# Kernel tuning notes

Measured on AMD Instinct MI355X. Metric: run time of the kernel, lower is better.

The kernel has to match this reference:

```python
import jax, jax.numpy as jnp
import numpy as np
from jax import lax

STRIDES = (8, 16, 32, 64, 128)
LEVEL_HW = ((100, 128), (50, 64), (25, 32), (13, 16), (7, 8))
NUM_CLASSES = 80
PRE_NMS_THRESH = 0.05
PRE_NMS_TOPK = 1000
NMS_THRESH = 0.6
MAX_DET = 100
CLS_OFFSET = 1.0e4  # > max image coordinate, separates classes for joint NMS


def setup_inputs() -> dict:
    key = jax.random.key(0)
    B = 16
    ks = jax.random.split(key, 3 * len(LEVEL_HW))
    inp = {}
    i = 0
    for lvl, (h, w) in enumerate(LEVEL_HW):
        # shift logits down so sigmoid scores are mostly below the 0.05 candidate
        # threshold (realistic detection sparsity)
        inp[f"logits_p{lvl + 3}"] = jax.random.normal(ks[i], (B, NUM_CLASSES, h, w), jnp.float32) - 4.0; i += 1
        inp[f"bbox_p{lvl + 3}"] = jax.random.uniform(ks[i], (B, 4, h, w), jnp.float32, minval=0.0, maxval=64.0); i += 1
        inp[f"ctr_p{lvl + 3}"] = jax.random.normal(ks[i], (B, 1, h, w), jnp.float32); i += 1
    inp["im_info"] = jnp.tile(jnp.array([[800.0, 1024.0]], jnp.float32), (B, 1))
    return inp


def _locations(h, w, stride):
    # FCOSLocation: center of each stride cell -> [HW, 2] as (x, y)
    sx = jnp.arange(w, dtype=jnp.float32) * stride + stride // 2
    sy = jnp.arange(h, dtype=jnp.float32) * stride + stride // 2
    yy, xx = jnp.meshgrid(sy, sx, indexing="ij")
    return jnp.stack([xx.reshape(-1), yy.reshape(-1)], axis=-1)


def _nms_single(boxes, scores, classes):
    # boxes [K,4], scores [K] (descending), classes [K] int
    off = classes.astype(jnp.float32)[:, None] * CLS_OFFSET
    nb = boxes + off  # class-offset trick -> per-class NMS in one pass
    areas = jnp.maximum(nb[:, 2] - nb[:, 0], 0.0) * jnp.maximum(nb[:, 3] - nb[:, 1], 0.0)

    def body(sc, _):
        i = jnp.argmax(sc)
        s = sc[i]
        bi = nb[i]
        xx1 = jnp.maximum(bi[0], nb[:, 0])
        yy1 = jnp.maximum(bi[1], nb[:, 1])
        xx2 = jnp.minimum(bi[2], nb[:, 2])
        yy2 = jnp.minimum(bi[3], nb[:, 3])
        inter = jnp.maximum(xx2 - xx1, 0.0) * jnp.maximum(yy2 - yy1, 0.0)
        iou = inter / (areas[i] + areas - inter + 1e-9)
        sc2 = jnp.where(iou >= NMS_THRESH, -jnp.inf, sc).at[i].set(-jnp.inf)
        return sc2, (i, s > 0.0)

    _, (idxs, valid) = lax.scan(body, scores, None, length=MAX_DET)
    det = jnp.concatenate(
        [boxes[idxs], scores[idxs][:, None], classes[idxs].astype(jnp.float32)[:, None]],
        axis=-1,
    )  # [MAX_DET, 6] = x1,y1,x2,y2,score,class
    return jnp.where(valid[:, None], det, 0.0)


def _forward(logits_p3, bbox_p3, ctr_p3, logits_p4, bbox_p4, ctr_p4,
             logits_p5, bbox_p5, ctr_p5, logits_p6, bbox_p6, ctr_p6,
             logits_p7, bbox_p7, ctr_p7, im_info):
    levels = [(logits_p3, bbox_p3, ctr_p3), (logits_p4, bbox_p4, ctr_p4),
              (logits_p5, bbox_p5, ctr_p5), (logits_p6, bbox_p6, ctr_p6),
              (logits_p7, bbox_p7, ctr_p7)]
    scores_l, boxes_l = [], []
    for (lg, rg, ct), stride in zip(levels, STRIDES):
        B, C, H, W = lg.shape
        cls = jax.nn.sigmoid(lg).transpose(0, 2, 3, 1).reshape(B, H * W, C)
        cen = jax.nn.sigmoid(ct).transpose(0, 2, 3, 1).reshape(B, H * W, 1)
        # candidate threshold on raw class prob, then modulate by centerness
        comb = jnp.where(cls > PRE_NMS_THRESH, cls * cen, 0.0)
        locs = _locations(H, W, stride)  # [HW, 2]
        reg = rg.transpose(0, 2, 3, 1).reshape(B, H * W, 4)  # (l, t, r, b)
        bx = jnp.stack([locs[None, :, 0] - reg[..., 0],
                        locs[None, :, 1] - reg[..., 1],
                        locs[None, :, 0] + reg[..., 2],
                        locs[None, :, 1] + reg[..., 3]], axis=-1)
        scores_l.append(comb)
        boxes_l.append(bx)
    scores = jnp.concatenate(scores_l, axis=1)  # [B, N, C]
    boxes = jnp.concatenate(boxes_l, axis=1)    # [B, N, 4]
    B, N, C = scores.shape
    vals, idx = lax.top_k(scores.reshape(B, N * C), PRE_NMS_TOPK)  # [B, K]
    loc = idx // C
    cls_id = idx % C
    cand = jnp.take_along_axis(boxes, loc[..., None], axis=1)  # [B, K, 4]
    h = im_info[:, 0:1]
    w = im_info[:, 1:2]
    x1 = jnp.clip(cand[..., 0], 0.0, w - 1.0)
    y1 = jnp.clip(cand[..., 1], 0.0, h - 1.0)
    x2 = jnp.clip(cand[..., 2], 0.0, w - 1.0)
    y2 = jnp.clip(cand[..., 3], 0.0, h - 1.0)
    cand = jnp.stack([x1, y1, x2, y2], axis=-1)
    sc = jnp.where(vals > 0.0, jnp.sqrt(jnp.maximum(vals, 0.0) + 1e-12), 0.0)
    return jax.vmap(_nms_single)(cand, sc, cls_id)  # [B, MAX_DET, 6]


def reference(logits_p3, bbox_p3, ctr_p3, logits_p4, bbox_p4, ctr_p4,
              logits_p5, bbox_p5, ctr_p5, logits_p6, bbox_p6, ctr_p6,
              logits_p7, bbox_p7, ctr_p7, im_info):
    return _forward(logits_p3, bbox_p3, ctr_p3, logits_p4, bbox_p4, ctr_p4,
                    logits_p5, bbox_p5, ctr_p5, logits_p6, bbox_p6, ctr_p6,
                    logits_p7, bbox_p7, ctr_p7, im_info)
```

## Files before the change

kernel.cpp:

```cpp
#include <hip/hip_runtime.h>
#include <math.h>

#pragma clang fp contract(off)

#define NB 16
#define NC 80
#define NTOT 17064
#define TOPK 1000
#define NBINS 8192
#define CAP 4096
#define MAXDET 100
#define CNTSTRIDE 64
#define CHUNK 128
#define GH 128
#define WSEGCAP 256
#define FB 16

struct Ptrs {
    const float* lg[5];
    const float* bb[5];
    const float* ct[5];
};

__device__ __forceinline__ void level_of(int n, int& l, int& hw, int& W,
                                         int& stride, int& half, int& HW) {
    if (n < 12800)      { l = 0; hw = n;         W = 128; stride = 8;   half = 4;  HW = 12800; }
    else if (n < 16000) { l = 1; hw = n - 12800; W = 64;  stride = 16;  half = 8;  HW = 3200;  }
    else if (n < 16800) { l = 2; hw = n - 16000; W = 32;  stride = 32;  half = 16; HW = 800;   }
    else if (n < 17008) { l = 3; hw = n - 16800; W = 16;  stride = 64;  half = 32; HW = 208;   }
    else                { l = 4; hw = n - 17008; W = 8;   stride = 128; half = 64; HW = 56;    }
}

__device__ __forceinline__ float fast_sig(float x) {
    float e = __expf(-x);
    return __builtin_amdgcn_rcpf(1.0f + e);
}

#define HG_EMIT(BITS, NN, CC, POS)                                            \
    {                                                                         \
        int lb = (int)(((BITS) - 32u) >> 19) - BINBASE;                       \
        lb = (lb < 0) ? 0 : ((lb > 63) ? 63 : lb);                            \
        atomicAdd(&whv[lb], 1u);             \
        unsigned pos_ = (POS);                                                \
        if (pos_ < WSEGCAP) {                                                 \
            unsigned idx_ = (unsigned)((NN) * NC + (CC));                     \
            segw[pos_] = ((unsigned long long)(BITS) << 32) | idx_;           \
        }                                                                     \
    }

#define LOADQ(I, V, C, HWV, CCV)                                              \
    V = make_float4(-40.f, -40.f, -40.f, -40.f);                              \
    C = make_float4(0.f, 0.f, 0.f, 0.f);                                      \
    HWV = 0; CCV = 0;                                                         \
    if ((I) < NF4) {                                                          \
        CCV = (I) / HW4; HWV = (I) - CCV * HW4;                               \
        V = *(const float4*)(lgb + (size_t)(I) * 4);                          \
        C = *(const float4*)(ctb + HWV * 4);                                  \
    }

template<int HW4, int NF4, int LVOFF>
__device__ __forceinline__ void histg_level(const float* lgb, const float* ctb,
        int tid, int bx, int gx, unsigned FB_LO, int BINBASE, unsigned* whv,
        unsigned& wcnt, unsigned long long* segw, unsigned long long ltmask) {
    const int stride = gx * 512;
    int i0 = bx * 512;
    if (i0 >= NF4) return;
    float4 va, vb, ca, cb;
    int hwa, hwb, cca, ccb;
    LOADQ(i0 + tid, va, ca, hwa, cca)
    LOADQ(i0 + 256 + tid, vb, cb, hwb, ccb)
    for (; i0 < NF4; ) {
        int in0 = i0 + stride;
        float4 nva, nvb, nca, ncb;
        int nhwa, nhwb, ncca, nccb;
        LOADQ(in0 + tid, nva, nca, nhwa, ncca)
        LOADQ(in0 + 256 + tid, nvb, ncb, nhwb, nccb)
        unsigned b0 = __float_as_uint(fast_sig(va.x) * fast_sig(ca.x));
        unsigned b1 = __float_as_uint(fast_sig(va.y) * fast_sig(ca.y));
        unsigned b2 = __float_as_uint(fast_sig(va.z) * fast_sig(ca.z));
        unsigned b3 = __float_as_uint(fast_sig(va.w) * fast_sig(ca.w));
        unsigned b4 = __float_as_uint(fast_sig(vb.x) * fast_sig(cb.x));
        unsigned b5 = __float_as_uint(fast_sig(vb.y) * fast_sig(cb.y));
        unsigned b6 = __float_as_uint(fast_sig(vb.z) * fast_sig(cb.z));
        unsigned b7 = __float_as_uint(fast_sig(vb.w) * fast_sig(cb.w));
        bool f0 = b0 >= FB_LO, f1 = b1 >= FB_LO, f2 = b2 >= FB_LO, f3 = b3 >= FB_LO;
        bool f4 = b4 >= FB_LO, f5 = b5 >= FB_LO, f6 = b6 >= FB_LO, f7 = b7 >= FB_LO;
        unsigned long long m0 = __ballot(f0), m1 = __ballot(f1);
        unsigned long long m2 = __ballot(f2), m3 = __ballot(f3);
        unsigned long long m4 = __ballot(f4), m5 = __ballot(f5);
        unsigned long long m6 = __ballot(f6), m7 = __ballot(f7);
        if (m0 | m1 | m2 | m3 | m4 | m5 | m6 | m7) {
            unsigned t0 = (unsigned)__popcll(m0), t1 = (unsigned)__popcll(m1);
            unsigned t2 = (unsigned)__popcll(m2), t3 = (unsigned)__popcll(m3);
            unsigned t4 = (unsigned)__popcll(m4), t5 = (unsigned)__popcll(m5);
            unsigned t6 = (unsigned)__popcll(m6), t7 = (unsigned)__popcll(m7);
            unsigned wb = wcnt;
            wcnt = wb + t0 + t1 + t2 + t3 + t4 + t5 + t6 + t7;
            int nb0a = LVOFF + hwa * 4, nb0b = LVOFF + hwb * 4;
            if (f0) HG_EMIT(b0, nb0a + 0, cca, wb + (unsigned)__popcll(m0 & ltmask))
            if (f1) HG_EMIT(b1, nb0a + 1, cca, wb + t0 + (unsigned)__popcll(m1 & ltmask))
            if (f2) HG_EMIT(b2, nb0a + 2, cca, wb + t0 + t1 + (unsigned)__popcll(m2 & ltmask))
            if (f3) HG_EMIT(b3, nb0a + 3, cca, wb + t0 + t1 + t2 + (unsigned)__popcll(m3 & ltmask))
            if (f4) HG_EMIT(b4, nb0b + 0, ccb, wb + t0 + t1 + t2 + t3 + (unsigned)__popcll(m4 & ltmask))
            if (f5) HG_EMIT(b5, nb0b + 1, ccb, wb + t0 + t1 + t2 + t3 + t4 + (unsigned)__popcll(m5 & ltmask))
            if (f6) HG_EMIT(b6, nb0b + 2, ccb, wb + t0 + t1 + t2 + t3 + t4 + t5 + (unsigned)__popcll(m6 & ltmask))
            if (f7) HG_EMIT(b7, nb0b + 3, ccb, wb + t0 + t1 + t2 + t3 + t4 + t5 + t6 + (unsigned)__popcll(m7 & ltmask))
        }
        i0 = in0;
        va = nva; ca = nca; hwa = nhwa; cca = ncca;
        vb = nvb; cb = ncb; hwb = nhwb; ccb = nccb;
    }
}
#undef LOADQ
#undef HG_EMIT

__global__ void __launch_bounds__(256) k_histB(Ptrs p, unsigned* hist, unsigned* cnt2,
                                               unsigned* wavecnt, unsigned long long* segs) {
    __shared__ unsigned wh[4][64];
    int b = blockIdx.y, tid = threadIdx.x, bx = blockIdx.x, gx = gridDim.x;
    int wv = tid >> 6, lane = tid & 63;
    if (bx == 0 && tid == 0) cnt2[(size_t)b * CNTSTRIDE] = 0;
    ((unsigned*)wh)[tid] = 0;
    unsigned FB_LO = __float_as_uint(0.08f) - 64u;
    int BINBASE = (int)(__float_as_uint(0.08f) >> 19);
    unsigned* whv = wh[wv];
    unsigned long long ltmask = (1ULL << lane) - 1ULL;
    unsigned wcnt = 0;
    unsigned long long* segw = segs + (((size_t)b * GH + bx) * 4 + wv) * WSEGCAP;

    histg_level<3200, 256000,     0>(p.lg[0] + (size_t)b * NC * 12800, p.ct[0] + (size_t)b * 12800, tid, bx, gx, FB_LO, BINBASE, whv, wcnt, segw, ltmask);
    histg_level< 800,  64000, 12800>(p.lg[1] + (size_t)b * NC * 3200,  p.ct[1] + (size_t)b * 3200,  tid, bx, gx, FB_LO, BINBASE, whv, wcnt, segw, ltmask);
    histg_level< 200,  16000, 16000>(p.lg[2] + (size_t)b * NC * 800,   p.ct[2] + (size_t)b * 800,   tid, bx, gx, FB_LO, BINBASE, whv, wcnt, segw, ltmask);
    histg_level<  52,   4160, 16800>(p.lg[3] + (size_t)b * NC * 208,   p.ct[3] + (size_t)b * 208,   tid, bx, gx, FB_LO, BINBASE, whv, wcnt, segw, ltmask);
    histg_level<  14,   1120, 17008>(p.lg[4] + (size_t)b * NC * 56,    p.ct[4] + (size_t)b * 56,    tid, bx, gx, FB_LO, BINBASE, whv, wcnt, segw, ltmask);

    if (lane == 0)
        wavecnt[((size_t)b * GH + bx) * 4 + wv] = wcnt;
    __syncthreads();
    if (tid < 64) {
        unsigned s = wh[0][tid] + wh[1][tid] + wh[2][tid] + wh[3][tid];
        hist[((size_t)b * GH + bx) * 64 + tid] = s;
    }
}

template<int HW4, int NF4>
__device__ __forceinline__ void histf_level(const float* lgb, const float* ctb,
                                            int tid, unsigned* hist) {
    for (int i0 = 0; i0 < NF4; i0 += 256) {
        int i = i0 + tid;
        if (i < NF4) {
            int c = i / HW4, hwf = i - c * HW4;
            float4 v = *(const float4*)(lgb + c * (HW4 * 4) + hwf * 4);
            if (v.x > -2.95f || v.y > -2.95f || v.z > -2.95f || v.w > -2.95f) {
                float4 cv = *(const float4*)(ctb + hwf * 4);
                float xs[4] = {v.x, v.y, v.z, v.w};
                float cs[4] = {cv.x, cv.y, cv.z, cv.w};
#pragma unroll
                for (int j = 0; j < 4; ++j) {
                    float x = xs[j];
                    if (x > -2.95f) {
                        float cls = fast_sig(x);
                        if (cls > 0.04999f) {
                            bool in = true;
                            if (cls < 0.05001f)
                                in = (1.0f / (1.0f + expf(-x))) > 0.05f;
                            if (in) {
                                float cen = fast_sig(cs[j]);
                                unsigned bits = __float_as_uint(cls * cen);
                                unsigned cb = (bits > 32u) ? bits - 32u : 0u;
                                atomicAdd(&hist[cb >> 19], 1u);
                            }
                        }
                    }
                }
            }
        }
    }
}

#define CD_J(J, X, CT, NB0, CC, F, K)                                         \
    if ((X) > xpre) {                                                         \
        float cls = 1.0f / (1.0f + expf(-(X)));                               \
        if (cls > 0.05f) {                                                    \
            float cen = 1.0f / (1.0f + expf(-(CT)));                          \
            float comb = cls * cen;                                           \
            unsigned bits = __float_as_uint(comb);                            \
            if ((bits >> 19) >= Tb) {                                         \
                unsigned idx = (unsigned)(((NB0) + (J)) * NC + (CC));         \
                K = ((unsigned long long)bits << 32) | (0xFFFFFFFFu - idx);   \
                F = true;                                                     \
            }                                                                 \
        }                                                                     \
    }

template<int HW4, int NF4, int LVOFF>
__device__ __forceinline__ void compact_level(const float* lgb, const float* ctb,
        int tid, int lane, int bx, int gx, unsigned Tb, float xpre,
        unsigned* cntb, unsigned long long* selb, unsigned long long ltmask) {
    for (int i0 = bx * 512; i0 < NF4; i0 += gx * 512) {
        int ia = i0 + tid, ib2 = i0 + 256 + tid;
        bool la = ia < NF4, lb2 = ib2 < NF4;
        float4 va = make_float4(-9.f, -9.f, -9.f, -9.f);
        float4 vb = make_float4(-9.f, -9.f, -9.f, -9.f);
        int hwa = 0, hwb = 0, cca = 0, ccb = 0;
        if (la) {
            cca = ia / HW4; hwa = ia - cca * HW4;
            va = *(const float4*)(lgb + cca * (HW4 * 4) + hwa * 4);
        }
        if (lb2) {
            ccb = ib2 / HW4; hwb = ib2 - ccb * HW4;
            vb = *(const float4*)(lgb + ccb * (HW4 * 4) + hwb * 4);
        }
        {
            bool f0 = false, f1 = false, f2 = false, f3 = false;
            unsigned long long k0 = 0, k1 = 0, k2 = 0, k3 = 0;
            if (va.x > xpre || va.y > xpre || va.z > xpre || va.w > xpre) {
                float4 cv = *(const float4*)(ctb + hwa * 4);
                int nb0 = LVOFF + hwa * 4;
                CD_J(0, va.x, cv.x, nb0, cca, f0, k0)
                CD_J(1, va.y, cv.y, nb0, cca, f1, k1)
                CD_J(2, va.z, cv.z, nb0, cca, f2, k2)
                CD_J(3, va.w, cv.w, nb0, cca, f3, k3)
            }
            unsigned long long m0 = __ballot(f0), m1 = __ballot(f1);
            unsigned long long m2 = __ballot(f2), m3 = __ballot(f3);
            if (m0 | m1 | m2 | m3) {
                unsigned t0 = (unsigned)__popcll(m0), t1 = (unsigned)__popcll(m1);
                unsigned t2 = (unsigned)__popcll(m2), t3 = (unsigned)__popcll(m3);
                int basep = 0;
                if (lane == 0) basep = (int)atomicAdd(cntb, t0 + t1 + t2 + t3);
                basep = __shfl(basep, 0);
                if (f0) { int pos = basep + (int)__popcll(m0 & ltmask);                       if (pos < CAP) selb[pos] = k0; }
                if (f1) { int pos = basep + (int)t0 + (int)__popcll(m1 & ltmask);             if (pos < CAP) selb[pos] = k1; }
                if (f2) { int pos = basep + (int)(t0 + t1) + (int)__popcll(m2 & ltmask);      if (pos < CAP) selb[pos] = k2; }
                if (f3) { int pos = basep + (int)(t0 + t1 + t2) + (int)__popcll(m3 & ltmask); if (pos < CAP) selb[pos] = k3; }
            }
        }
        {
            bool f0 = false, f1 = false, f2 = false, f3 = false;
            unsigned long long k0 = 0, k1 = 0, k2 = 0, k3 = 0;
            if (vb.x > xpre || vb.y > xpre || vb.z > xpre || vb.w > xpre) {
                float4 cv = *(const float4*)(ctb + hwb * 4);
                int nb0 = LVOFF + hwb * 4;
                CD_J(0, vb.x, cv.x, nb0, ccb, f0, k0)
                CD_J(1, vb.y, cv.y, nb0, ccb, f1, k1)
                CD_J(2, vb.z, cv.z, nb0, ccb, f2, k2)
                CD_J(3, vb.w, cv.w, nb0, ccb, f3, k3)
            }
            unsigned long long m0 = __ballot(f0), m1 = __ballot(f1);
            unsigned long long m2 = __ballot(f2), m3 = __ballot(f3);
            if (m0 | m1 | m2 | m3) {
                unsigned t0 = (unsigned)__popcll(m0), t1 = (unsigned)__popcll(m1);
                unsigned t2 = (unsigned)__popcll(m2), t3 = (unsigned)__popcll(m3);
                int basep = 0;
                if (lane == 0) basep = (int)atomicAdd(cntb, t0 + t1 + t2 + t3);
                basep = __shfl(basep, 0);
                if (f0) { int pos = basep + (int)__popcll(m0 & ltmask);                       if (pos < CAP) selb[pos] = k0; }
                if (f1) { int pos = basep + (int)t0 + (int)__popcll(m1 & ltmask);             if (pos < CAP) selb[pos] = k1; }
                if (f2) { int pos = basep + (int)(t0 + t1) + (int)__popcll(m2 & ltmask);      if (pos < CAP) selb[pos] = k2; }
                if (f3) { int pos = basep + (int)(t0 + t1 + t2) + (int)__popcll(m3 & ltmask); if (pos < CAP) selb[pos] = k3; }
            }
        }
    }
}
#undef CD_J

__device__ __forceinline__ void run_compact(const Ptrs& p, int b, int tid, int lane,
        int bx, int gx, unsigned Tb, unsigned* cnt2, unsigned long long* sel) {
    float mthr = __uint_as_float(Tb << 19);
    float xpre = -2.95f;
    if (mthr > 1e-37f && mthr < 1.0f) {
        float lm = logf(mthr / (1.0f - mthr)) - 0.01f;
        if (lm > xpre) xpre = lm;
    }
    unsigned long long ltmask = (1ULL << lane) - 1ULL;
    unsigned* cntb = cnt2 + (size_t)b * CNTSTRIDE;
    unsigned long long* selb = sel + (size_t)b * CAP;
    compact_level<3200, 256000,     0>(p.lg[0] + (size_t)b * NC * 12800, p.ct[0] + (size_t)b * 12800, tid, lane, bx, gx, Tb, xpre, cntb, selb, ltmask);
    compact_level< 800,  64000, 12800>(p.lg[1] + (size_t)b * NC * 3200,  p.ct[1] + (size_t)b * 3200,  tid, lane, bx, gx, Tb, xpre, cntb, selb, ltmask);
    compact_level< 200,  16000, 16000>(p.lg[2] + (size_t)b * NC * 800,   p.ct[2] + (size_t)b * 800,   tid, lane, bx, gx, Tb, xpre, cntb, selb, ltmask);
    compact_level<  52,   4160, 16800>(p.lg[3] + (size_t)b * NC * 208,   p.ct[3] + (size_t)b * 208,   tid, lane, bx, gx, Tb, xpre, cntb, selb, ltmask);
    compact_level<  14,   1120, 17008>(p.lg[4] + (size_t)b * NC * 56,    p.ct[4] + (size_t)b * 56,    tid, lane, bx, gx, Tb, xpre, cntb, selb, ltmask);
}

__global__ void __launch_bounds__(256) k_filter(Ptrs p, const unsigned* hist,
        const unsigned* wavecnt, const unsigned long long* segs,
        unsigned* cnt2, unsigned long long* sel) {
    __shared__ unsigned part[4][64];
    __shared__ unsigned red[64];
    __shared__ unsigned fullh[NBINS];
    __shared__ int s_T, s_ok;
    __shared__ unsigned s_ovf;
    int b = blockIdx.y, tid = threadIdx.x, bx = blockIdx.x;
    int bin = tid & 63, grp = tid >> 6, lane = tid & 63, wv = tid >> 6;
    int BINBASE = (int)(__float_as_uint(0.08f) >> 19);

    unsigned s = 0;
    for (int blk = grp; blk < GH; blk += 4)
        s += hist[((size_t)b * GH + blk) * 64 + bin];
    part[grp][bin] = s;
    if (tid == 0) s_ovf = 0;
    __syncthreads();
    if (tid < 64) red[tid] = part[0][tid] + part[1][tid] + part[2][tid] + part[3][tid];
    unsigned ov = 0;
    for (int i = tid; i < GH * 4; i += 256)
        ov |= (wavecnt[(size_t)b * GH * 4 + i] > WSEGCAP) ? 1u : 0u;
    if (ov) atomicOr(&s_ovf, 1u);
    __syncthreads();
    if (tid == 0) {
        unsigned suf1 = 0;
        for (int i = 1; i < 64; ++i) suf1 += red[i];
        unsigned run = 0; int Tl = 0;
        for (int i = 63; i >= 1; --i) {
            run += red[i];
            if (run >= TOPK) { Tl = i; break; }
        }
        s_ok = (suf1 >= TOPK);
        s_T = Tl + BINBASE;
    }
    __syncthreads();

    if (s_ok && !s_ovf) {
        unsigned Tb = (unsigned)s_T;
        unsigned FLO = (Tb << 19) - 64u;
        unsigned* cntb = cnt2 + (size_t)b * CNTSTRIDE;
        unsigned long long* selb = sel + (size_t)b * CAP;
        unsigned long long ltmask = (1ULL << lane) - 1ULL;
        for (int sg = bx * 4 + wv; sg < GH * 4; sg += FB * 4) {
            unsigned cs = wavecnt[(size_t)b * GH * 4 + sg];
            if (cs > WSEGCAP) cs = WSEGCAP;
            const unsigned long long* sp = segs + ((size_t)b * GH * 4 + sg) * WSEGCAP;
            for (unsigned e0 = 0; e0 < cs; e0 += 64) {
                unsigned e = e0 + (unsigned)lane;
                bool take = false;
                unsigned long long key = 0;
                if (e < cs) {
                    unsigned long long kk = sp[e];
                    if ((unsigned)(kk >> 32) >= FLO) {
                        unsigned idx = (unsigned)kk;
                        int n = (int)(idx / NC), c = (int)(idx - (unsigned)n * NC);
                        int l, hw, W, stride, half, HW;
                        level_of(n, l, hw, W, stride, half, HW);
                        float x   = p.lg[l][(size_t)b * NC * HW + (size_t)c * HW + hw];
                        float ctv = p.ct[l][(size_t)b * HW + hw];
                        float cls = 1.0f / (1.0f + expf(-x));
                        if (cls > 0.05f) {
                            float cen = 1.0f / (1.0f + expf(-ctv));
                            unsigned bits = __float_as_uint(cls * cen);
                            if ((bits >> 19) >= Tb) {
                                key = ((unsigned long long)bits << 32) | (0xFFFFFFFFu - idx);
                                take = true;
                            }
                        }
                    }
                }
                unsigned long long m = __ballot(take);
                if (m) {
                    unsigned tot = (unsigned)__popcll(m);
                    int basep = 0;
                    if (lane == 0) basep = (int)atomicAdd(cntb, tot);
                    basep = __shfl(basep, 0);
                    if (take) {
                        int pos = basep + (int)__popcll(m & ltmask);
                        if (pos < CAP) selb[pos] = key;
                    }
                }
            }
        }
        return;
    }

    if (!s_ok) {
        if (bx != 0) return;
        for (int i = tid; i < NBINS; i += 256) fullh[i] = 0;
        __syncthreads();
        histf_level<3200, 256000>(p.lg[0] + (size_t)b * NC * 12800, p.ct[0] + (size_t)b * 12800, tid, fullh);
        histf_level< 800,  64000>(p.lg[1] + (size_t)b * NC * 3200,  p.ct[1] + (size_t)b * 3200,  tid, fullh);
        histf_level< 200,  16000>(p.lg[2] + (size_t)b * NC * 800,   p.ct[2] + (size_t)b * 800,   tid, fullh);
        histf_level<  52,   4160>(p.lg[3] + (size_t)b * NC * 208,   p.ct[3] + (size_t)b * 208,   tid, fullh);
        histf_level<  14,   1120>(p.lg[4] + (size_t)b * NC * 56,    p.ct[4] + (size_t)b * 56,    tid, fullh);
        __syncthreads();
        if (tid == 0) {
            unsigned run = 0; int Tf = 0;
            for (int i = NBINS - 1; i >= 0; --i) {
                run += fullh[i];
                if (run >= TOPK) { Tf = i; break; }
            }
            s_T = Tf;
        }
        __syncthreads();
        run_compact(p, b, tid, lane, 0, 1, (unsigned)s_T, cnt2, sel);
        return;
    }

    run_compact(p, b, tid, lane, bx, FB, (unsigned)s_T, cnt2, sel);
}

__global__ void __launch_bounds__(256) k_rankdec(Ptrs p, const unsigned* cnt,
                                                 const unsigned long long* sel,
                                                 const float* im_info, float* cand) {
    __shared__ __align__(16) unsigned long long keys[CAP];
    int b = blockIdx.y, tid = threadIdx.x;
    unsigned M = cnt[(size_t)b * CNTSTRIDE];
    if (M > CAP) M = CAP;
    int s0 = blockIdx.x * 256;
    if (s0 >= (int)M) return;
    int Mpad = (int)((M + 1u) & ~1u);
    for (int i = tid; i < Mpad; i += 256)
        keys[i] = (i < (int)M) ? sel[(size_t)b * CAP + i] : 0ULL;
    __syncthreads();

    int s = s0 + tid;
    if (s >= (int)M) return;
    unsigned long long k = keys[s];
    int rank = 0;
    for (int j = 0; j < Mpad; j += 2) {
        ulonglong2 kk = *(const ulonglong2*)&keys[j];
        rank += (kk.x > k) ? 1 : 0;
        rank += (kk.y > k) ? 1 : 0;
    }
    if (rank >= TOPK) return;

    float Him = im_info[b * 2 + 0], Wim = im_info[b * 2 + 1];
    float xmax = Wim - 1.0f, ymax = Him - 1.0f;
    unsigned sb = (unsigned)(k >> 32);
    unsigned idx = 0xFFFFFFFFu - (unsigned)(k & 0xFFFFFFFFu);
    float val = __uint_as_float(sb);
    int n = idx / NC, c = idx - n * NC;
    int l, hw, W, stride, half, HW;
    level_of(n, l, hw, W, stride, half, HW);
    int wx = hw % W, hy = hw / W;
    float locx = (float)(wx * stride + half);
    float locy = (float)(hy * stride + half);
    const float* bb = p.bb[l] + (size_t)b * 4 * HW + hw;
    float r0 = bb[0], r1 = bb[(size_t)HW], r2 = bb[(size_t)2 * HW], r3 = bb[(size_t)3 * HW];
    float x1 = locx - r0, y1 = locy - r1, x2 = locx + r2, y2 = locy + r3;
    x1 = fminf(fmaxf(x1, 0.f), xmax);
    y1 = fminf(fmaxf(y1, 0.f), ymax);
    x2 = fminf(fmaxf(x2, 0.f), xmax);
    y2 = fminf(fmaxf(y2, 0.f), ymax);
    float scv = sqrtf(val + 1e-12f);
    float off = (float)c * 10000.0f;
    float a0 = x1 + off, a1 = y1 + off, a2 = x2 + off, a3 = y2 + off;
    float area = fmaxf(a2 - a0, 0.f) * fmaxf(a3 - a1, 0.f);
    float* dst = cand + ((size_t)b * TOPK + rank) * 12;
    *(float4*)(dst + 0) = make_float4(x1, y1, x2, y2);
    *(float4*)(dst + 4) = make_float4(a0, a1, a2, a3);
    *(float4*)(dst + 8) = make_float4(area, scv, (float)c, 0.f);
}

__global__ void __launch_bounds__(64) k_nms(const unsigned* cnt, const float* cand,
                                            float* out) {
    __shared__ float4 s_ob[CHUNK], s_nb[CHUNK], s_ms[CHUNK];
    int b = blockIdx.x, lane = threadIdx.x;
    unsigned M = cnt[(size_t)b * CNTSTRIDE];
    if (M > CAP) M = CAP;
    int ncand = (int)M < TOPK ? (int)M : TOPK;
    const float* src = cand + (size_t)b * TOPK * 12;
    float* ob = out + (size_t)b * MAXDET * 6;

    int na = 0;
    float4 a0b = make_float4(0.f, 0.f, 0.f, 0.f);
    float4 a1b = make_float4(0.f, 0.f, 0.f, 0.f);
    float a0a = 0.f, a1a = 0.f;

    for (int base = 0; base < ncand && na < MAXDET; base += CHUNK) {
        int cn = ncand - base; if (cn > CHUNK) cn = CHUNK;
        for (int cidx = lane; cidx < cn; cidx += 64) {
            const float* s = src + (size_t)(base + cidx) * 12;
            s_ob[cidx] = *(const float4*)(s + 0);
            s_nb[cidx] = *(const float4*)(s + 4);
            s_ms[cidx] = *(const float4*)(s + 8);
        }
        __syncthreads();
        for (int r = 0; r < cn && na < MAXDET; ++r) {
            float4 cb = s_nb[r];
            float ca = s_ms[r].x;
            bool sup = false;
            if (lane < na) {
                float xx1 = fmaxf(a0b.x, cb.x);
                float yy1 = fmaxf(a0b.y, cb.y);
                float xx2 = fminf(a0b.z, cb.z);
                float yy2 = fminf(a0b.w, cb.w);
                float inter = fmaxf(xx2 - xx1, 0.f) * fmaxf(yy2 - yy1, 0.f);
                float iou = inter / (((a0a + ca) - inter) + 1e-9f);
                sup = (iou >= 0.6f);
            }
            if (lane + 64 < na) {
                float xx1 = fmaxf(a1b.x, cb.x);
                float yy1 = fmaxf(a1b.y, cb.y);
                float xx2 = fminf(a1b.z, cb.z);
                float yy2 = fminf(a1b.w, cb.w);
                float inter = fmaxf(xx2 - xx1, 0.f) * fmaxf(yy2 - yy1, 0.f);
                float iou = inter / (((a1a + ca) - inter) + 1e-9f);
                sup |= (iou >= 0.6f);
            }
            if (__ballot(sup) == 0ULL) {
                if (lane == (na & 63)) {
                    if (na < 64) { a0b = cb; a0a = ca; }
                    else         { a1b = cb; a1a = ca; }
                }
                if (lane == 0) {
                    float4 o4 = s_ob[r]; float4 m4 = s_ms[r];
                    ob[na * 6 + 0] = o4.x; ob[na * 6 + 1] = o4.y;
                    ob[na * 6 + 2] = o4.z; ob[na * 6 + 3] = o4.w;
                    ob[na * 6 + 4] = m4.y; ob[na * 6 + 5] = m4.z;
                }
                ++na;
            }
        }
        __syncthreads();
    }
    for (int q = na * 6 + lane; q < MAXDET * 6; q += 64)
        ob[q] = 0.f;
}

extern "C" void kernel_launch(void* const* d_in, const int* in_sizes, int n_in,
                              void* d_out, int out_size, void* d_ws, size_t ws_size,
                              hipStream_t stream) {
    Ptrs p;
    for (int l = 0; l < 5; ++l) {
        p.lg[l] = (const float*)d_in[3 * l + 0];
        p.bb[l] = (const float*)d_in[3 * l + 1];
        p.ct[l] = (const float*)d_in[3 * l + 2];
    }
    const float* im_info = (const float*)d_in[15];
    float* out = (float*)d_out;
    unsigned char* w = (unsigned char*)d_ws;

    unsigned* hist           = (unsigned*)(w);
    unsigned* cnt2           = (unsigned*)(w + 524288);
    unsigned* wavecnt        = (unsigned*)(w + 528384);
    unsigned long long* segs = (unsigned long long*)(w + 561152);
    unsigned long long* sel  = (unsigned long long*)(w + 17338368);
    float* cand              = (float*)(w + 17862656);

    k_histB<<<dim3(GH, NB), 256, 0, stream>>>(p, hist, cnt2, wavecnt, segs);
    k_filter<<<dim3(FB, NB), 256, 0, stream>>>(p, hist, wavecnt, segs, cnt2, sel);
    k_rankdec<<<dim3(16, NB), 256, 0, stream>>>(p, cnt2, sel, im_info, cand);
    k_nms<<<NB, 64, 0, stream>>>(cnt2, cand, out);
}
```

Before: 229.7 us.

## Precompute pairwise IoU suppression bitmask in parallel, then run bitmask-based greedy NMS

Replaces the serial per-candidate IoU-against-accepted-boxes loop with a separate kernel that computes the full upper-triangular IoU suppression bitmask across many blocks. The NMS kernel then walks candidates in order and ORs mask rows into a removal set. This moves the arithmetic out of the single-wave serial loop, at the cost of computing all pairwise IoUs and an extra launch plus mask traffic. The greedy loop still scans every candidate serially, now with LDS reads.

```diff
diff --git a/kernel.cpp b/kernel.cpp
--- a/kernel.cpp
+++ b/kernel.cpp
@@ -11,10 +11,10 @@
 #define CAP 4096
 #define MAXDET 100
 #define CNTSTRIDE 64
-#define CHUNK 128
 #define GH 128
 #define WSEGCAP 256
 #define FB 16
+#define NROWS 1024
 
 struct Ptrs {
     const float* lg[5];
@@ -449,67 +449,89 @@
     *(float4*)(dst + 8) = make_float4(area, scv, (float)c, 0.f);
 }
 
-__global__ void __launch_bounds__(64) k_nms(const unsigned* cnt, const float* cand,
-                                            float* out) {
-    __shared__ float4 s_ob[CHUNK], s_nb[CHUNK], s_ms[CHUNK];
+__global__ void __launch_bounds__(256) k_iou(const unsigned* cnt, const float* cand,
+                                             unsigned long long* mask) {
+    __shared__ float4 s_cb[64];
+    __shared__ float s_ca[64];
+    int b = blockIdx.z, ct = blockIdx.x, tid = threadIdx.x;
+    unsigned M = cnt[(size_t)b * CNTSTRIDE];
+    if (M > CAP) M = CAP;
+    int ncand = (int)M < TOPK ? (int)M : TOPK;
+    const float* src = cand + (size_t)b * TOPK * 12;
+    int jbase = ct * 64;
+    if (tid < 64) {
+        int j = jbase + tid;
+        if (j < ncand) {
+            s_cb[tid] = *(const float4*)(src + (size_t)j * 12 + 4);
+            s_ca[tid] = src[(size_t)j * 12 + 8];
+        } else {
+            s_cb[tid] = make_float4(0.f, 0.f, 0.f, 0.f);
+            s_ca[tid] = 0.f;
+        }
+    }
+    __syncthreads();
+    int r = blockIdx.y * 256 + tid;
+    if (r >= ncand) return;
+    float4 rb = *(const float4*)(src + (size_t)r * 12 + 4);
+    float ra = src[(size_t)r * 12 + 8];
+    unsigned long long word = 0;
+#pragma unroll 4
+    for (int j0 = 0; j0 < 64; ++j0) {
+        int j = jbase + j0;
+        if (j > r && j < ncand) {
+            float4 cb = s_cb[j0];
+            float ca = s_ca[j0];
+            float xx1 = fmaxf(rb.x, cb.x);
+            float yy1 = fmaxf(rb.y, cb.y);
+            float xx2 = fminf(rb.z, cb.z);
+            float yy2 = fminf(rb.w, cb.w);
+            float inter = fmaxf(xx2 - xx1, 0.f) * fmaxf(yy2 - yy1, 0.f);
+            float iou = inter / (((ra + ca) - inter) + 1e-9f);
+            if (iou >= 0.6f) word |= 1ULL << j0;
+        }
+    }
+    mask[((size_t)b * NROWS + r) * 16 + ct] = word;
+}
+
+__global__ void __launch_bounds__(64) k_nms(const unsigned* cnt,
+                                            const unsigned long long* mask,
+                                            const float* cand, float* out) {
+    __shared__ unsigned long long s_rows[64][16];
+    __shared__ unsigned long long s_remv[16];
+    __shared__ int s_acc[MAXDET];
     int b = blockIdx.x, lane = threadIdx.x;
     unsigned M = cnt[(size_t)b * CNTSTRIDE];
     if (M > CAP) M = CAP;
     int ncand = (int)M < TOPK ? (int)M : TOPK;
     const float* src = cand + (size_t)b * TOPK * 12;
     float* ob = out + (size_t)b * MAXDET * 6;
-
+    const unsigned long long* mb = mask + (size_t)b * NROWS * 16;
+    if (lane < 16) s_remv[lane] = 0ULL;
     int na = 0;
-    float4 a0b = make_float4(0.f, 0.f, 0.f, 0.f);
-    float4 a1b = make_float4(0.f, 0.f, 0.f, 0.f);
-    float a0a = 0.f, a1a = 0.f;
-
-    for (int base = 0; base < ncand && na < MAXDET; base += CHUNK) {
-        int cn = ncand - base; if (cn > CHUNK) cn = CHUNK;
-        for (int cidx = lane; cidx < cn; cidx += 64) {
-            const float* s = src + (size_t)(base + cidx) * 12;
-            s_ob[cidx] = *(const float4*)(s + 0);
-            s_nb[cidx] = *(const float4*)(s + 4);
-            s_ms[cidx] = *(const float4*)(s + 8);
-        }
+    for (int base = 0; base < ncand && na < MAXDET; base += 64) {
+        int cn = ncand - base; if (cn > 64) cn = 64;
+        for (int t = lane; t < cn * 16; t += 64)
+            s_rows[t >> 4][t & 15] = mb[(size_t)(base + (t >> 4)) * 16 + (t & 15)];
         __syncthreads();
-        for (int r = 0; r < cn && na < MAXDET; ++r) {
-            float4 cb = s_nb[r];
-            float ca = s_ms[r].x;
-            bool sup = false;
-            if (lane < na) {
-                float xx1 = fmaxf(a0b.x, cb.x);
-                float yy1 = fmaxf(a0b.y, cb.y);
-                float xx2 = fminf(a0b.z, cb.z);
-                float yy2 = fminf(a0b.w, cb.w);
-                float inter = fmaxf(xx2 - xx1, 0.f) * fmaxf(yy2 - yy1, 0.f);
-                float iou = inter / (((a0a + ca) - inter) + 1e-9f);
-                sup = (iou >= 0.6f);
-            }
-            if (lane + 64 < na) {
-                float xx1 = fmaxf(a1b.x, cb.x);
-                float yy1 = fmaxf(a1b.y, cb.y);
-                float xx2 = fminf(a1b.z, cb.z);
-                float yy2 = fminf(a1b.w, cb.w);
-                float inter = fmaxf(xx2 - xx1, 0.f) * fmaxf(yy2 - yy1, 0.f);
-                float iou = inter / (((a1a + ca) - inter) + 1e-9f);
-                sup |= (iou >= 0.6f);
-            }
-            if (__ballot(sup) == 0ULL) {
-                if (lane == (na & 63)) {
-                    if (na < 64) { a0b = cb; a0a = ca; }
-                    else         { a1b = cb; a1a = ca; }
-                }
-                if (lane == 0) {
-                    float4 o4 = s_ob[r]; float4 m4 = s_ms[r];
-                    ob[na * 6 + 0] = o4.x; ob[na * 6 + 1] = o4.y;
-                    ob[na * 6 + 2] = o4.z; ob[na * 6 + 3] = o4.w;
-                    ob[na * 6 + 4] = m4.y; ob[na * 6 + 5] = m4.z;
-                }
+        int cw = base >> 6;
+        unsigned long long curw = s_remv[cw];
+        for (int r = 0; r < cn; ++r) {
+            if (!((curw >> r) & 1ULL)) {
+                curw |= s_rows[r][cw];
+                if (lane < 16) s_remv[lane] |= s_rows[r][lane];
+                if (lane == 0) s_acc[na] = base + r;
                 ++na;
+                if (na == MAXDET) break;
             }
         }
         __syncthreads();
+    }
+    for (int q = lane; q < na; q += 64) {
+        int rr = s_acc[q];
+        const float* s = src + (size_t)rr * 12;
+        ob[q * 6 + 0] = s[0]; ob[q * 6 + 1] = s[1];
+        ob[q * 6 + 2] = s[2]; ob[q * 6 + 3] = s[3];
+        ob[q * 6 + 4] = s[9]; ob[q * 6 + 5] = s[10];
     }
     for (int q = na * 6 + lane; q < MAXDET * 6; q += 64)
         ob[q] = 0.f;
@@ -534,9 +556,11 @@
     unsigned long long* segs = (unsigned long long*)(w + 561152);
     unsigned long long* sel  = (unsigned long long*)(w + 17338368);
     float* cand              = (float*)(w + 17862656);
+    unsigned long long* maskb = (unsigned long long*)(w + 18630656);
 
     k_histB<<<dim3(GH, NB), 256, 0, stream>>>(p, hist, cnt2, wavecnt, segs);
     k_filter<<<dim3(FB, NB), 256, 0, stream>>>(p, hist, wavecnt, segs, cnt2, sel);
     k_rankdec<<<dim3(16, NB), 256, 0, stream>>>(p, cnt2, sel, im_info, cand);
-    k_nms<<<NB, 64, 0, stream>>>(cnt2, cand, out);
-}
+    k_iou<<<dim3(16, 4, NB), 256, 0, stream>>>(cnt2, cand, maskb);
+    k_nms<<<NB, 64, 0, stream>>>(cnt2, maskb, cand, out);
+}
```

Result: slower. 241.1 us (+5.0%).
